# Kernel tuning notes

Measured on AMD Instinct MI355X. Metric: run time of the kernel, lower is better.

The kernel has to match this reference:

```python
import jax, jax.numpy as jnp
import numpy as np

SCORE_THRESHOLD = 0.05
NMS_THRESHOLD = 0.6
MAX_DETECTIONS = 300


def setup_inputs() -> dict:
    key = jax.random.key(0)
    kb, kc, kn = jax.random.split(key, 3)
    B, N, C = 8, 50000, 16
    # build well-formed (x1, y1, x2, y2) boxes so IoU is meaningful
    u = jax.random.uniform(kb, (B, N, 4), dtype=jnp.float32)
    x1 = u[..., 0] * 900.0
    y1 = u[..., 1] * 900.0
    x2 = x1 + 5.0 + u[..., 2] * 120.0
    y2 = y1 + 5.0 + u[..., 3] * 120.0
    boxes = jnp.stack([x1, y1, x2, y2], axis=-1)
    classification = jax.random.uniform(kc, (B, N, C), dtype=jnp.float32)
    # keep centerness strictly positive so sqrt is smooth and kept scores are > 0
    centerness = jax.random.uniform(kn, (B, N, 1), dtype=jnp.float32) * 0.9 + 0.1
    return {"boxes": boxes, "classification": classification, "centerness": centerness}


def _iou_one_vs_all(box, boxes):
    # box: [4], boxes: [N,4] in (x1,y1,x2,y2).  IoU is invariant to the x/y swap
    # the TF code does before tf.image.non_max_suppression.
    ix1 = jnp.maximum(box[0], boxes[:, 0])
    iy1 = jnp.maximum(box[1], boxes[:, 1])
    ix2 = jnp.minimum(box[2], boxes[:, 2])
    iy2 = jnp.minimum(box[3], boxes[:, 3])
    inter = jnp.maximum(ix2 - ix1, 0.0) * jnp.maximum(iy2 - iy1, 0.0)
    area = (box[2] - box[0]) * (box[3] - box[1])
    areas = (boxes[:, 2] - boxes[:, 0]) * (boxes[:, 3] - boxes[:, 1])
    return inter / (area + areas - inter + 1e-8)


def _detect_image(boxes, cls, cent):
    # boxes [N,4], cls [N,C], cent [N,1]
    N, C = cls.shape
    combined = jnp.sqrt(cls * cent)                         # [N,C] sqrt(score*centerness)
    # per-class NMS candidates: score_threshold applied to the RAW class score
    nms_scores = jnp.where(cls > SCORE_THRESHOLD, combined, -1.0).T   # [C,N]
    # the greedy-NMS keep mask is discrete: no gradient flows through it
    nms_scores = jax.lax.stop_gradient(nms_scores)
    boxes_ng = jax.lax.stop_gradient(boxes)

    def nms_one_class(s):
        def step(s, _):
            i = jnp.argmax(s)
            keep = s[i] > 0.0
            iou = _iou_one_vs_all(boxes_ng[i], boxes_ng)
            s_new = jnp.where(iou > NMS_THRESHOLD, -1.0, s).at[i].set(-1.0)
            return jnp.where(keep, s_new, s), (i, keep)
        _, (idxs, keeps) = jax.lax.scan(step, s, None, length=MAX_DETECTIONS)
        # scatter kept picks into a [N] bool mask (keeps=False entries are no-ops)
        return jnp.zeros(s.shape[0], dtype=bool).at[idxs].max(keeps)

    kept = jax.vmap(nms_one_class)(nms_scores)              # [C,N]
    # global top-k over all surviving (class, anchor) pairs, sentinel -1 for dropped
    flat = jnp.where(kept, combined.T, -1.0).reshape(-1)    # [C*N]
    top_s, top_i = jax.lax.top_k(flat, MAX_DETECTIONS)
    label = top_i // N
    anchor = top_i % N
    valid = top_s > 0.0
    out_boxes = jnp.where(valid[:, None], boxes[anchor], -1.0)   # [300,4], pad=-1
    out_scores = jnp.where(valid, top_s, -1.0)                   # [300],   pad=-1
    out_labels = jnp.where(valid, label, -1).astype(jnp.int32)   # [300],   pad=-1
    return out_boxes, out_scores, out_labels


def reference(boxes, classification, centerness):
    return jax.vmap(_detect_image)(boxes, classification, centerness)
```

## Files before the change

### kernel.cpp

```cpp
#include <hip/hip_runtime.h>
#include <cstdint>
#include <cstddef>

#define MAXDET 300
#define IOU_THR 0.6f
#define SCORE_THR 0.05f
#define T0 0.9f
#define CAP 2048
#define SCAN 512
#define LCAP 64
#define SPLIT 128
#define BS 1024
#define NBUCK 1024
#define KEYS_MAX 576
#define BITS_BASE 0x3F666666u

typedef unsigned int u32;
typedef unsigned long long u64;


__global__ __launch_bounds__(256) void score_compact_kernel(
    const float* __restrict__ cls, const float* __restrict__ cent,
    int N, int C,
    u64* __restrict__ candPacked, int* __restrict__ cntRaw, int* __restrict__ totalCand)
{
    const int b = blockIdx.x / SPLIT;
    const int s = blockIdx.x % SPLIT;
    const int chunk = (N + SPLIT - 1) / SPLIT;
    const int n0 = s * chunk;
    const int n1 = min(n0 + chunk, N);
    const int tid = threadIdx.x;
    const int q  = tid & 3;
    const int ar = tid >> 2;

    __shared__ int lcnt[16];
    __shared__ int ltot[16];
    __shared__ int lbase[16];
    __shared__ u64 lbuf[16][LCAP];

    if (tid < 16) { lcnt[tid] = 0; ltot[tid] = 0; }
    __syncthreads();

    int myTot[4] = {0, 0, 0, 0};
    for (int n = n0 + ar; n < n1; n += 64) {
        const float4 r = *reinterpret_cast<const float4*>(
            cls + ((size_t)b * N + n) * 16 + q * 4);
        const float ce = cent[(size_t)b * N + n];
        const float cv[4] = {r.x, r.y, r.z, r.w};
#pragma unroll
        for (int u = 0; u < 4; ++u) {
            const float v = cv[u];
            if (v > SCORE_THR) {
                myTot[u]++;
                const float prod = v * ce;
                if (prod >= 0.80f) {
                    const float comb = sqrtf(prod);
                    if (comb >= T0) {
                        const int c = 4 * q + u;
                        const u64 key = ((u64)__float_as_uint(comb) << 32)
                                      | (u32)(0xFFFFFFFFu - (u32)n);
                        const int lp = atomicAdd(&lcnt[c], 1);
                        if (lp < LCAP) {
                            lbuf[c][lp] = key;
                        } else {
                            const int pos = atomicAdd(&cntRaw[b * 16 + c], 1);
                            if (pos < CAP)
                                candPacked[((size_t)(b * 16 + c) << 11) + pos] = key;
                        }
                    }
                }
            }
        }
    }
#pragma unroll
    for (int u = 0; u < 4; ++u) atomicAdd(&ltot[4 * q + u], myTot[u]);
    __syncthreads();

    if (tid < 16) {
        const int m = min(lcnt[tid], LCAP);
        lbase[tid] = atomicAdd(&cntRaw[b * 16 + tid], m);
        atomicAdd(&totalCand[b * 16 + tid], ltot[tid]);
    }
    __syncthreads();

    for (int idx = tid; idx < 16 * LCAP; idx += 256) {
        const int c = idx >> 6;
        const int k = idx & 63;
        if (k < min(lcnt[c], LCAP)) {
            const int pos = lbase[c] + k;
            if (pos < CAP)
                candPacked[((size_t)(b * 16 + c) << 11) + pos] = lbuf[c][k];
        }
    }
}

__global__ __launch_bounds__(1024)
__attribute__((amdgpu_waves_per_eu(4, 4)))
void sort_nms_kernel(
    const float* __restrict__ boxes, const u64* __restrict__ candPacked,
    const int* __restrict__ cntRaw, const int* __restrict__ totalCand,
    int N, int C,
    int* __restrict__ keptIdx, float* __restrict__ keptScore,
    int* __restrict__ keptCnt, int* __restrict__ flagInc)
{
    const int bc  = blockIdx.x;
    const int b   = bc / C;
    const int tid = threadIdx.x;
    const int wv  = tid >> 6;
    const int ln  = tid & 63;
    const int raw = cntRaw[bc];
    const int use = min(raw, CAP);
    const int scanN = min(use, SCAN);
    const float* __restrict__ boxb = boxes + (size_t)b * N * 4;
    const u64* __restrict__ gbase = candPacked + ((size_t)bc << 11);

    __shared__ u64    keyS[KEYS_MAX];
    __shared__ float4 sbox4[SCAN];
    __shared__ float  sar[SCAN];
    __shared__ int    scA[NBUCK];
    __shared__ int    scB[NBUCK];
    __shared__ int    wsum[16];
    __shared__ u64    mask[SCAN][9];
    __shared__ float  ksc[MAXDET];
    __shared__ int    kix[MAXDET];
    __shared__ int    cntSh, flagSh;

    scA[tid] = 0;
    if (tid == 0) flagSh = 0;
    __syncthreads();

    u64 k0 = 0, k1 = 0; int bk0 = -1, bk1 = -1, r0 = 0, r1 = 0;
    if (tid < use) {
        k0 = gbase[tid];
        const u32 bits = (u32)(k0 >> 32);
        const u32 d = bits > BITS_BASE ? bits - BITS_BASE : 0u;
        bk0 = (NBUCK - 1) - (int)min(d >> 11, (u32)(NBUCK - 1));
        r0 = atomicAdd(&scA[bk0], 1);
    }
    if (tid + 1024 < use) {
        k1 = gbase[tid + 1024];
        const u32 bits = (u32)(k1 >> 32);
        const u32 d = bits > BITS_BASE ? bits - BITS_BASE : 0u;
        bk1 = (NBUCK - 1) - (int)min(d >> 11, (u32)(NBUCK - 1));
        r1 = atomicAdd(&scA[bk1], 1);
    }
    __syncthreads();

    const int own = scA[tid];
    int inc = own;
#pragma unroll
    for (int d = 1; d < 64; d <<= 1) {
        const int t = __shfl_up(inc, d);
        if (ln >= d) inc += t;
    }
    if (ln == 63) wsum[wv] = inc;
    __syncthreads();
    if (wv == 0) {
        int v = (ln < 16) ? wsum[ln] : 0;
#pragma unroll
        for (int d = 1; d < 16; d <<= 1) {
            const int t = __shfl_up(v, d);
            if (ln >= d) v += t;
        }
        if (ln < 16) wsum[ln] = v;
    }
    __syncthreads();
    const int wbase  = (wv == 0) ? 0 : wsum[wv - 1];
    const int myBase = wbase + inc - own;
    scB[tid] = myBase;
    __syncthreads();
    int* const bbase = scB;

    if (bk0 >= 0) { const int p = bbase[bk0] + r0; if (p < KEYS_MAX) keyS[p] = k0; }
    if (bk1 >= 0) { const int p = bbase[bk1] + r1; if (p < KEYS_MAX) keyS[p] = k1; }
    if (own > 0 && myBase < SCAN && myBase + own > KEYS_MAX) flagSh = 1;
    __syncthreads();

    {
        const int lo = myBase;
        const int hi = min(lo + own, KEYS_MAX);
        if (own >= 2 && lo < KEYS_MAX) {
            for (int a = lo + 1; a < hi; ++a) {
                const u64 kk = keyS[a];
                int p = a - 1;
                while (p >= lo && keyS[p] < kk) { keyS[p + 1] = keyS[p]; --p; }
                keyS[p + 1] = kk;
            }
        }
    }
    __syncthreads();

    if (tid < scanN) {
        const u64 kk = keyS[tid];
        const int n = (int)(0xFFFFFFFFu - (u32)kk);
        const float4 bx = *reinterpret_cast<const float4*>(boxb + (size_t)n * 4);
        sbox4[tid] = bx;
        sar[tid]   = (bx.z - bx.x) * (bx.w - bx.y);
    }
    __syncthreads();

    {
        float rjx1[8], rjy1[8], rjx2[8], rjy2[8], rja[8];
#pragma unroll
        for (int w = 0; w < 8; ++w) {
            const int j = w * 64 + ln;
            const float4 bj = sbox4[j];
            rjx1[w] = bj.x; rjy1[w] = bj.y; rjx2[w] = bj.z; rjy2[w] = bj.w;
            rja[w]  = sar[j];
            asm volatile("" : "+v"(rjx1[w]), "+v"(rjy1[w]), "+v"(rjx2[w]),
                              "+v"(rjy2[w]), "+v"(rja[w]));
        }
        for (int i = wv; i < scanN; i += 16) {
            const float4 bp = sbox4[i];
            const float pa = sar[i];
            const int wlo = i >> 6;
#pragma unroll
            for (int w = 0; w < 8; ++w) {
                if (w >= wlo) {
                    const int j = w * 64 + ln;
                    const bool jv = (j < scanN) && (j != i);
                    const float ix1 = fmaxf(bp.x, rjx1[w]), iy1 = fmaxf(bp.y, rjy1[w]);
                    const float ix2 = fminf(bp.z, rjx2[w]), iy2 = fminf(bp.w, rjy2[w]);
                    const bool ov = jv && (ix2 > ix1) && (iy2 > iy1);
                    bool sup = false;
                    if (__any(ov)) {
                        const float inter = fmaxf(ix2 - ix1, 0.f) * fmaxf(iy2 - iy1, 0.f);
                        const float iou = inter / (pa + rja[w] - inter + 1e-8f);
                        sup = ov && (iou > IOU_THR);
                    }
                    const u64 bal = __ballot(sup);
                    if (ln == 0) mask[i][w] = bal;
                }
            }
        }
    }
    __syncthreads();

    if (wv == 0) {
        u64 remv[8] = {0, 0, 0, 0, 0, 0, 0, 0};
        int cnt = 0;
#pragma unroll
        for (int c = 0; c < 8; ++c) {
            if (cnt < MAXDET) {
                const int i = c * 64 + ln;
                const bool valid = (i < scanN);
                u64 alive = __ballot(valid && !((remv[c] >> ln) & 1ULL));
                const u64 sub = valid ? mask[i][c] : 0ULL;
                u64 keptM = 0ULL;
                const int cbase = cnt;
                while (alive) {
                    const int f = __ffsll((unsigned long long)alive) - 1;
                    keptM |= (1ULL << f);
                    ++cnt;
                    if (cnt >= MAXDET) break;
                    const bool meSup = ((sub >> f) & 1ULL) != 0ULL;
                    const u64 supM = __ballot(meSup);
                    alive &= ~(supM | (1ULL << f));
                }
                if ((keptM >> ln) & 1ULL) {
                    const int pos = cbase + __popcll(keptM & ((1ULL << ln) - 1ULL));
                    const u64 kk = keyS[i];
                    ksc[pos] = __uint_as_float((u32)(kk >> 32));
                    kix[pos] = (int)(0xFFFFFFFFu - (u32)kk);
                }
                if (cnt < MAXDET && c < 7) {
#pragma unroll
                    for (int w = 0; w < 8; ++w) {
                        if (w > c) {
                            u64 x = ((keptM >> ln) & 1ULL) ? mask[c * 64 + ln][w] : 0ULL;
#pragma unroll
                            for (int m = 1; m < 64; m <<= 1)
                                x |= (u64)__shfl_xor((long long)x, m);
                            remv[w] |= x;
                        }
                    }
                }
            }
        }
        if (ln == 0) cntSh = cnt;
    }
    __syncthreads();

    const int cnt = cntSh;
    for (int k2 = tid; k2 < cnt; k2 += 1024) {
        keptIdx[bc * MAXDET + k2]   = kix[k2];
        keptScore[bc * MAXDET + k2] = ksc[k2];
    }
    if (tid == 0) {
        keptCnt[bc] = cnt;
        flagInc[bc] = (raw > CAP
                       || flagSh
                       || (cnt < MAXDET && totalCand[bc] > use)
                       || (cnt < MAXDET && use > scanN)
                      ) ? 1 : 0;
    }
}


__device__ __forceinline__ void combineMax(float& bs, int& bi, float os, int oi) {
    if (os > bs || (os == bs && oi < bi)) { bs = os; bi = oi; }
}

template<int NPT>
__global__ __launch_bounds__(BS) void nms_slow_kernel(
    const float* __restrict__ boxes, const float* __restrict__ cls,
    const float* __restrict__ cent, int B, int N, int C,
    int* __restrict__ keptIdx, float* __restrict__ keptScore, int* __restrict__ keptCnt,
    const int* __restrict__ flagInc)
{
    const int bc = blockIdx.x;
    if (flagInc != nullptr && flagInc[bc] == 0) return;
    const int b   = bc / C;
    const int c   = bc - b * C;
    const int tid = threadIdx.x;

    const float* __restrict__ clsb  = cls  + (size_t)b * N * C + c;
    const float* __restrict__ centb = cent + (size_t)b * N;
    const float* __restrict__ boxb  = boxes + (size_t)b * N * 4;

    float s[NPT];
#pragma unroll
    for (int j = 0; j < NPT; ++j) {
        int n = tid + j * BS;
        float v = -1.0f;
        if (n < N) {
            float cv = clsb[(size_t)n * C];
            if (cv > SCORE_THR) v = sqrtf(cv * centb[n]);
        }
        s[j] = v;
    }

    __shared__ float kx1[MAXDET], ky1[MAXDET], kx2[MAXDET], ky2[MAXDET];
    __shared__ float kscore[MAXDET];
    __shared__ int   kidx[MAXDET];
    __shared__ float redS[BS / 64];
    __shared__ int   redI[BS / 64];
    __shared__ float pbox[4];
    __shared__ float pscoreSh;
    __shared__ int   ctrl;
    __shared__ int   supFlag;

    const int lane = tid & 63;
    const int wid  = tid >> 6;
    const int NW   = BS / 64;
    int cnt = 0;

    const int maxIter = N + MAXDET + 2;
    for (int iter = 0; iter < maxIter; ++iter) {
        float bs = -1.0f; int bi = 0x7fffffff;
#pragma unroll
        for (int j = 0; j < NPT; ++j) {
            if (s[j] > bs) { bs = s[j]; bi = tid + j * BS; }
        }
        for (int m = 1; m < 64; m <<= 1) {
            float os = __shfl_xor(bs, m);
            int   oi = __shfl_xor(bi, m);
            combineMax(bs, bi, os, oi);
        }
        if (lane == 0) { redS[wid] = bs; redI[wid] = bi; }
        __syncthreads();
        if (tid == 0) {
            float gs = redS[0]; int gi = redI[0];
            for (int w = 1; w < NW; ++w) combineMax(gs, gi, redS[w], redI[w]);
            supFlag = 0;
            if (gs <= 0.0f) {
                ctrl = -1;
            } else {
                ctrl = gi; pscoreSh = gs;
                const float4 bx = *reinterpret_cast<const float4*>(boxb + (size_t)gi * 4);
                pbox[0] = bx.x; pbox[1] = bx.y; pbox[2] = bx.z; pbox[3] = bx.w;
            }
        }
        __syncthreads();
        const int P = ctrl;
        if (P < 0) break;

        if ((P & (BS - 1)) == tid) {
            const int jp = P >> 10;
#pragma unroll
            for (int j = 0; j < NPT; ++j) if (j == jp) s[j] = -1.0f;
        }

        if (tid < cnt) {
            const float px1 = pbox[0], py1 = pbox[1], px2 = pbox[2], py2 = pbox[3];
            const float qx1 = kx1[tid], qy1 = ky1[tid], qx2 = kx2[tid], qy2 = ky2[tid];
            const float ix1 = fmaxf(qx1, px1), iy1 = fmaxf(qy1, py1);
            const float ix2 = fminf(qx2, px2), iy2 = fminf(qy2, py2);
            const float inter = fmaxf(ix2 - ix1, 0.0f) * fmaxf(iy2 - iy1, 0.0f);
            const float aq = (qx2 - qx1) * (qy2 - qy1);
            const float ap = (px2 - px1) * (py2 - py1);
            const float iou = inter / (aq + ap - inter + 1e-8f);
            if (iou > IOU_THR) supFlag = 1;
        }
        __syncthreads();
        if (supFlag == 0) {
            if (tid == 0) {
                kx1[cnt] = pbox[0]; ky1[cnt] = pbox[1];
                kx2[cnt] = pbox[2]; ky2[cnt] = pbox[3];
                kscore[cnt] = pscoreSh; kidx[cnt] = P;
            }
            ++cnt;
            if (cnt == MAXDET) break;
        }
    }

    for (int k = tid; k < cnt; k += BS) {
        keptIdx[(size_t)bc * MAXDET + k]   = kidx[k];
        keptScore[(size_t)bc * MAXDET + k] = kscore[k];
    }
    if (tid == 0) keptCnt[bc] = cnt;
}

__global__ __launch_bounds__(1024) void topk_kernel(
    const float* __restrict__ boxes, const int* __restrict__ keptIdx,
    const float* __restrict__ keptScore, const int* __restrict__ keptCnt,
    int B, int N, int C, float* __restrict__ out)
{
    const int b   = blockIdx.x;
    const int tid = threadIdx.x;
    const int wv  = tid >> 6;
    const int ln  = tid & 63;

    __shared__ int cnts[16];
    __shared__ int cntA[NBUCK];
    __shared__ int bbS[NBUCK];
    __shared__ int wsum[16];
    __shared__ u32 wmin[16], wmax[16];
    __shared__ u64 sorted[16 * MAXDET];
    __shared__ int totalSh;

    if (tid < 16) cnts[tid] = (tid < C) ? keptCnt[b * C + tid] : 0;
    cntA[tid] = 0;
    __syncthreads();
    if (tid == 0) {
        int t = 0;
        for (int c = 0; c < C; ++c) t += cnts[c];
        totalSh = t;
    }

    const int TOT = C * MAXDET;
    u64 mk[5]; int mb[5], mr[5];
    u32 lmin = 0xFFFFFFFFu, lmax = 0u;
#pragma unroll
    for (int t = 0; t < 5; ++t) {
        mb[t] = -1;
        const int i = tid + t * 1024;
        if (i < TOT) {
            const int c = i / MAXDET;
            const int k = i - c * MAXDET;
            if (k < cnts[c]) {
                const float sc = keptScore[(b * C + c) * MAXDET + k];
                const u32 fl = (u32)(c * N + keptIdx[(b * C + c) * MAXDET + k]);
                mk[t] = ((u64)__float_as_uint(sc) << 32) | (0xFFFFFFFFu - fl);
                mb[t] = 0;
                const u32 bits = (u32)(mk[t] >> 32);
                lmin = min(lmin, bits);
                lmax = max(lmax, bits);
            }
        }
    }
#pragma unroll
    for (int m = 1; m < 64; m <<= 1) {
        lmin = min(lmin, (u32)__shfl_xor((int)lmin, m));
        lmax = max(lmax, (u32)__shfl_xor((int)lmax, m));
    }
    if (ln == 0) { wmin[wv] = lmin; wmax[wv] = lmax; }
    __syncthreads();
    u32 gmin = wmin[0], gmax = wmax[0];
#pragma unroll
    for (int w = 1; w < 16; ++w) { gmin = min(gmin, wmin[w]); gmax = max(gmax, wmax[w]); }
    const u64 range1 = (u64)(gmax - gmin) + 1;

#pragma unroll
    for (int t = 0; t < 5; ++t) {
        if (mb[t] == 0) {
            const u32 bits = (u32)(mk[t] >> 32);
            const int bk = (NBUCK - 1) - (int)(((u64)(bits - gmin) * NBUCK) / range1);
            mb[t] = bk;
            mr[t] = atomicAdd(&cntA[bk], 1);
        } else {
            mb[t] = -1;
        }
    }
    __syncthreads();

    const int own = cntA[tid];
    int inc = own;
#pragma unroll
    for (int d = 1; d < 64; d <<= 1) {
        const int t = __shfl_up(inc, d);
        if (ln >= d) inc += t;
    }
    if (ln == 63) wsum[wv] = inc;
    __syncthreads();
    if (wv == 0) {
        int v = (ln < 16) ? wsum[ln] : 0;
#pragma unroll
        for (int d = 1; d < 16; d <<= 1) {
            const int t = __shfl_up(v, d);
            if (ln >= d) v += t;
        }
        if (ln < 16) wsum[ln] = v;
    }
    __syncthreads();
    const int wbase  = (wv == 0) ? 0 : wsum[wv - 1];
    const int myBase = wbase + inc - own;
    bbS[tid] = myBase;
    __syncthreads();

#pragma unroll
    for (int t = 0; t < 5; ++t)
        if (mb[t] >= 0) sorted[bbS[mb[t]] + mr[t]] = mk[t];
    __syncthreads();

    {
        const int lo = myBase;
        const int hi = lo + own;
        if (own >= 2) {
            for (int a = lo + 1; a < hi; ++a) {
                const u64 kk = sorted[a];
                int p = a - 1;
                while (p >= lo && sorted[p] < kk) { sorted[p + 1] = sorted[p]; --p; }
                sorted[p + 1] = kk;
            }
        }
    }
    __syncthreads();

    const int total = totalSh;
    if (tid < MAXDET) {
        float4 bx = make_float4(-1.0f, -1.0f, -1.0f, -1.0f);
        float so = -1.0f, lo2 = -1.0f;
        if (tid < total) {
            const u64 kk = sorted[tid];
            so = __uint_as_float((u32)(kk >> 32));
            const int fl = (int)(0xFFFFFFFFu - (u32)kk);
            const int label  = fl / N;
            const int anchor = fl - label * N;
            bx = *reinterpret_cast<const float4*>(boxes + ((size_t)b * N + anchor) * 4);
            lo2 = (float)label;
        }
        *reinterpret_cast<float4*>(out + (size_t)(b * MAXDET + tid) * 4) = bx;
        out[(size_t)B * MAXDET * 4 + b * MAXDET + tid] = so;
        out[(size_t)B * MAXDET * 5 + b * MAXDET + tid] = lo2;
    }
}


extern "C" void kernel_launch(void* const* d_in, const int* in_sizes, int n_in,
                              void* d_out, int out_size, void* d_ws, size_t ws_size,
                              hipStream_t stream) {
    const float* boxes = (const float*)d_in[0];
    const float* cls   = (const float*)d_in[1];
    const float* cent  = (const float*)d_in[2];
    float* out = (float*)d_out;

    const int B = out_size / (MAXDET * 6);
    if (B <= 0) return;
    const int N = in_sizes[2] / B;
    const int C = in_sizes[1] / in_sizes[2];
    if (N <= 0 || C <= 0 || C > 16) return;
    const int BC = B * C;

    char* base = (char*)d_ws;
    size_t off = 0;
    int*   keptIdx   = (int*)(base + off);   off += (size_t)BC * MAXDET * sizeof(int);
    float* keptScore = (float*)(base + off); off += (size_t)BC * MAXDET * sizeof(float);
    int*   keptCnt   = (int*)(base + off);   off += (size_t)BC * sizeof(int);
    int*   flagInc   = (int*)(base + off);   off += (size_t)BC * sizeof(int);
    const size_t slowNeed = off;
    int*   cntRaw    = (int*)(base + off);   off += (size_t)BC * sizeof(int);
    int*   totalCand = (int*)(base + off);   off += (size_t)BC * sizeof(int);
    off = (off + 7) & ~(size_t)7;
    u64*   candPacked = (u64*)(base + off);  off += (size_t)BC * CAP * sizeof(u64);
    const size_t fastNeed = off;

    const int nptNeeded = (N + BS - 1) / BS;
    if (nptNeeded > 64) return;

    const bool fast = (C == 16) && (ws_size >= fastNeed);

    if (fast) {
        hipMemsetAsync(cntRaw, 0, 2 * (size_t)BC * sizeof(int), stream);
        score_compact_kernel<<<B * SPLIT, 256, 0, stream>>>(
            cls, cent, N, C, candPacked, cntRaw, totalCand);
        sort_nms_kernel<<<BC, 1024, 0, stream>>>(
            boxes, candPacked, cntRaw, totalCand, N, C,
            keptIdx, keptScore, keptCnt, flagInc);
        if (nptNeeded <= 49)
            nms_slow_kernel<49><<<BC, BS, 0, stream>>>(boxes, cls, cent, B, N, C,
                                                       keptIdx, keptScore, keptCnt, flagInc);
        else
            nms_slow_kernel<64><<<BC, BS, 0, stream>>>(boxes, cls, cent, B, N, C,
                                                       keptIdx, keptScore, keptCnt, flagInc);
    } else {
        if (ws_size < slowNeed) return;
        if (nptNeeded <= 49)
            nms_slow_kernel<49><<<BC, BS, 0, stream>>>(boxes, cls, cent, B, N, C,
                                                       keptIdx, keptScore, keptCnt, nullptr);
        else
            nms_slow_kernel<64><<<BC, BS, 0, stream>>>(boxes, cls, cent, B, N, C,
                                                       keptIdx, keptScore, keptCnt, nullptr);
    }

    topk_kernel<<<B, 1024, 0, stream>>>(boxes, keptIdx, keptScore, keptCnt, B, N, C, out);
}
```

Baseline: 106.5 us.

## Split fused sort+NMS into sort-gather, parallel IoU mask, and resolve kernels

Replaces the single per-(batch,class) sort_nms kernel with three kernels. The first bucket-sorts candidates and gathers boxes and areas to global memory. The second computes a 512x512 suppression bitmask across 4 blocks per class. The third is a single-wave greedy resolve over that bitmask. This aims to spread the IoU work over more CUs instead of one block per class. In exchange it adds two kernel launches, extra global-memory round trips, and more workspace, and it falls back to the old path when the workspace is too small.

```diff
diff --git a/kernel.cpp b/kernel.cpp
--- a/kernel.cpp
+++ b/kernel.cpp
@@ -91,6 +91,219 @@
             if (pos < CAP)
                 candPacked[((size_t)(b * 16 + c) << 11) + pos] = lbuf[c][k];
         }
+    }
+}
+
+__global__ __launch_bounds__(1024) void sort_gather_kernel(
+    const float* __restrict__ boxes, const u64* __restrict__ candPacked,
+    const int* __restrict__ cntRaw, int N, int C,
+    u64* __restrict__ keysG, float4* __restrict__ boxG, float* __restrict__ areaG,
+    int* __restrict__ scanNG, int* __restrict__ straddleG)
+{
+    const int bc  = blockIdx.x;
+    const int b   = bc / C;
+    const int tid = threadIdx.x;
+    const int wv  = tid >> 6;
+    const int ln  = tid & 63;
+    const int raw = cntRaw[bc];
+    const int use = min(raw, CAP);
+    const int scanN = min(use, SCAN);
+    const float* __restrict__ boxb = boxes + (size_t)b * N * 4;
+    const u64* __restrict__ gbase = candPacked + ((size_t)bc << 11);
+
+    __shared__ u64 keyS[KEYS_MAX];
+    __shared__ int scA[NBUCK];
+    __shared__ int scB[NBUCK];
+    __shared__ int wsum[16];
+    __shared__ int flagSh;
+
+    scA[tid] = 0;
+    if (tid == 0) flagSh = 0;
+    __syncthreads();
+
+    u64 k0 = 0, k1 = 0; int bk0 = -1, bk1 = -1, r0 = 0, r1 = 0;
+    if (tid < use) {
+        k0 = gbase[tid];
+        const u32 bits = (u32)(k0 >> 32);
+        const u32 d = bits > BITS_BASE ? bits - BITS_BASE : 0u;
+        bk0 = (NBUCK - 1) - (int)min(d >> 11, (u32)(NBUCK - 1));
+        r0 = atomicAdd(&scA[bk0], 1);
+    }
+    if (tid + 1024 < use) {
+        k1 = gbase[tid + 1024];
+        const u32 bits = (u32)(k1 >> 32);
+        const u32 d = bits > BITS_BASE ? bits - BITS_BASE : 0u;
+        bk1 = (NBUCK - 1) - (int)min(d >> 11, (u32)(NBUCK - 1));
+        r1 = atomicAdd(&scA[bk1], 1);
+    }
+    __syncthreads();
+
+    const int own = scA[tid];
+    int inc = own;
+#pragma unroll
+    for (int d = 1; d < 64; d <<= 1) {
+        const int t = __shfl_up(inc, d);
+        if (ln >= d) inc += t;
+    }
+    if (ln == 63) wsum[wv] = inc;
+    __syncthreads();
+    if (wv == 0) {
+        int v = (ln < 16) ? wsum[ln] : 0;
+#pragma unroll
+        for (int d = 1; d < 16; d <<= 1) {
+            const int t = __shfl_up(v, d);
+            if (ln >= d) v += t;
+        }
+        if (ln < 16) wsum[ln] = v;
+    }
+    __syncthreads();
+    const int wbase  = (wv == 0) ? 0 : wsum[wv - 1];
+    const int myBase = wbase + inc - own;
+    scB[tid] = myBase;
+    __syncthreads();
+    int* const bbase = scB;
+
+    if (bk0 >= 0) { const int p = bbase[bk0] + r0; if (p < KEYS_MAX) keyS[p] = k0; }
+    if (bk1 >= 0) { const int p = bbase[bk1] + r1; if (p < KEYS_MAX) keyS[p] = k1; }
+    if (own > 0 && myBase < SCAN && myBase + own > KEYS_MAX) flagSh = 1;
+    __syncthreads();
+
+    {
+        const int lo = myBase;
+        const int hi = min(lo + own, KEYS_MAX);
+        if (own >= 2 && lo < KEYS_MAX) {
+            for (int a = lo + 1; a < hi; ++a) {
+                const u64 kk = keyS[a];
+                int p = a - 1;
+                while (p >= lo && keyS[p] < kk) { keyS[p + 1] = keyS[p]; --p; }
+                keyS[p + 1] = kk;
+            }
+        }
+    }
+    __syncthreads();
+
+    if (tid < scanN) {
+        const u64 kk = keyS[tid];
+        const int n = (int)(0xFFFFFFFFu - (u32)kk);
+        const float4 bx = *reinterpret_cast<const float4*>(boxb + (size_t)n * 4);
+        keysG[(size_t)bc * SCAN + tid] = kk;
+        boxG[(size_t)bc * SCAN + tid]  = bx;
+        areaG[(size_t)bc * SCAN + tid] = (bx.z - bx.x) * (bx.w - bx.y);
+    }
+    if (tid == 0) { scanNG[bc] = scanN; straddleG[bc] = flagSh; }
+}
+
+__global__ __launch_bounds__(256) void mask_kernel(
+    const float4* __restrict__ boxG, const float* __restrict__ areaG,
+    const int* __restrict__ scanNG, u64* __restrict__ maskG)
+{
+    const int blk = blockIdx.x;
+    const int bc  = blk >> 2;
+    const int rr  = blk & 3;
+    const int scanN = scanNG[bc];
+    const int row0 = rr * 128;
+    if (row0 >= scanN) return;
+    const int tid = threadIdx.x;
+    const int wv  = tid >> 6;
+    const int ln  = tid & 63;
+    const size_t base = (size_t)bc * SCAN;
+
+    float rjx1[8], rjy1[8], rjx2[8], rjy2[8], rja[8];
+#pragma unroll
+    for (int w = 0; w < 8; ++w) {
+        const float4 bj = boxG[base + w * 64 + ln];
+        rjx1[w] = bj.x; rjy1[w] = bj.y; rjx2[w] = bj.z; rjy2[w] = bj.w;
+        rja[w]  = areaG[base + w * 64 + ln];
+    }
+
+    const int rowEnd = min(row0 + 128, scanN);
+    for (int i = row0 + wv; i < rowEnd; i += 4) {
+        const float4 bp = boxG[base + i];
+        const float pa  = areaG[base + i];
+        const int wlo = i >> 6;
+#pragma unroll
+        for (int w = 0; w < 8; ++w) {
+            if (w >= wlo) {
+                const int j = w * 64 + ln;
+                const bool jv = (j < scanN) && (j != i);
+                const float ix1 = fmaxf(bp.x, rjx1[w]), iy1 = fmaxf(bp.y, rjy1[w]);
+                const float ix2 = fminf(bp.z, rjx2[w]), iy2 = fminf(bp.w, rjy2[w]);
+                const bool ov = jv && (ix2 > ix1) && (iy2 > iy1);
+                bool sup = false;
+                if (__any(ov)) {
+                    const float inter = fmaxf(ix2 - ix1, 0.f) * fmaxf(iy2 - iy1, 0.f);
+                    const float iou = inter / (pa + rja[w] - inter + 1e-8f);
+                    sup = ov && (iou > IOU_THR);
+                }
+                const u64 bal = __ballot(sup);
+                if (ln == 0) maskG[(base + i) * 8 + w] = bal;
+            }
+        }
+    }
+}
+
+__global__ __launch_bounds__(64) void resolve_kernel(
+    const u64* __restrict__ keysG, const u64* __restrict__ maskG,
+    const int* __restrict__ cntRaw, const int* __restrict__ totalCand,
+    const int* __restrict__ scanNG, const int* __restrict__ straddleG,
+    int* __restrict__ keptIdx, float* __restrict__ keptScore,
+    int* __restrict__ keptCnt, int* __restrict__ flagInc)
+{
+    const int bc = blockIdx.x;
+    const int ln = threadIdx.x;
+    const int raw = cntRaw[bc];
+    const int use = min(raw, CAP);
+    const int scanN = scanNG[bc];
+    const size_t base = (size_t)bc * SCAN;
+
+    u64 remv[8] = {0, 0, 0, 0, 0, 0, 0, 0};
+    int cnt = 0;
+#pragma unroll
+    for (int c = 0; c < 8; ++c) {
+        if (cnt < MAXDET) {
+            const int i = c * 64 + ln;
+            const bool valid = (i < scanN);
+            u64 alive = __ballot(valid && !((remv[c] >> ln) & 1ULL));
+            const u64 sub = valid ? maskG[(base + i) * 8 + c] : 0ULL;
+            u64 keptM = 0ULL;
+            const int cbase = cnt;
+            while (alive) {
+                const int f = __ffsll((unsigned long long)alive) - 1;
+                keptM |= (1ULL << f);
+                ++cnt;
+                if (cnt >= MAXDET) break;
+                const bool meSup = ((sub >> f) & 1ULL) != 0ULL;
+                const u64 supM = __ballot(meSup);
+                alive &= ~(supM | (1ULL << f));
+            }
+            if ((keptM >> ln) & 1ULL) {
+                const int pos = cbase + __popcll(keptM & ((1ULL << ln) - 1ULL));
+                const u64 kk = keysG[base + i];
+                keptScore[bc * MAXDET + pos] = __uint_as_float((u32)(kk >> 32));
+                keptIdx[bc * MAXDET + pos]   = (int)(0xFFFFFFFFu - (u32)kk);
+            }
+            if (cnt < MAXDET && c < 7) {
+#pragma unroll
+                for (int w = 0; w < 8; ++w) {
+                    if (w > c) {
+                        u64 x = ((keptM >> ln) & 1ULL)
+                              ? maskG[(base + c * 64 + ln) * 8 + w] : 0ULL;
+#pragma unroll
+                        for (int m = 1; m < 64; m <<= 1)
+                            x |= (u64)__shfl_xor((long long)x, m);
+                        remv[w] |= x;
+                    }
+                }
+            }
+        }
+    }
+    if (ln == 0) {
+        keptCnt[bc] = cnt;
+        flagInc[bc] = (raw > CAP
+                       || straddleG[bc]
+                       || (cnt < MAXDET && totalCand[bc] > use)
+                       || (cnt < MAXDET && use > scanN)
+                      ) ? 1 : 0;
     }
 }
 
@@ -573,20 +786,38 @@
     int*   totalCand = (int*)(base + off);   off += (size_t)BC * sizeof(int);
     off = (off + 7) & ~(size_t)7;
     u64*   candPacked = (u64*)(base + off);  off += (size_t)BC * CAP * sizeof(u64);
-    const size_t fastNeed = off;
+    const size_t fusedNeed = off;
+    off = (off + 15) & ~(size_t)15;
+    float4* boxG   = (float4*)(base + off);  off += (size_t)BC * SCAN * sizeof(float4);
+    u64*    keysG  = (u64*)(base + off);     off += (size_t)BC * SCAN * sizeof(u64);
+    u64*    maskG  = (u64*)(base + off);     off += (size_t)BC * SCAN * 8 * sizeof(u64);
+    float*  areaG  = (float*)(base + off);   off += (size_t)BC * SCAN * sizeof(float);
+    int*    scanNG = (int*)(base + off);     off += (size_t)BC * sizeof(int);
+    int*    strG   = (int*)(base + off);     off += (size_t)BC * sizeof(int);
+    const size_t splitNeed = off;
 
     const int nptNeeded = (N + BS - 1) / BS;
     if (nptNeeded > 64) return;
 
-    const bool fast = (C == 16) && (ws_size >= fastNeed);
-
-    if (fast) {
+    const bool haveFast  = (C == 16) && (ws_size >= fusedNeed);
+    const bool haveSplit = (C == 16) && (ws_size >= splitNeed);
+
+    if (haveFast) {
         hipMemsetAsync(cntRaw, 0, 2 * (size_t)BC * sizeof(int), stream);
         score_compact_kernel<<<B * SPLIT, 256, 0, stream>>>(
             cls, cent, N, C, candPacked, cntRaw, totalCand);
-        sort_nms_kernel<<<BC, 1024, 0, stream>>>(
-            boxes, candPacked, cntRaw, totalCand, N, C,
-            keptIdx, keptScore, keptCnt, flagInc);
+        if (haveSplit) {
+            sort_gather_kernel<<<BC, 1024, 0, stream>>>(
+                boxes, candPacked, cntRaw, N, C, keysG, boxG, areaG, scanNG, strG);
+            mask_kernel<<<BC * 4, 256, 0, stream>>>(boxG, areaG, scanNG, maskG);
+            resolve_kernel<<<BC, 64, 0, stream>>>(
+                keysG, maskG, cntRaw, totalCand, scanNG, strG,
+                keptIdx, keptScore, keptCnt, flagInc);
+        } else {
+            sort_nms_kernel<<<BC, 1024, 0, stream>>>(
+                boxes, candPacked, cntRaw, totalCand, N, C,
+                keptIdx, keptScore, keptCnt, flagInc);
+        }
         if (nptNeeded <= 49)
             nms_slow_kernel<49><<<BC, BS, 0, stream>>>(boxes, cls, cent, B, N, C,
                                                        keptIdx, keptScore, keptCnt, flagInc);
```

Result: slower. 127.9 us (+20.1%).
